# Kernel tuning notes

Measured on AMD Instinct MI355X. Metric: run time of the kernel, lower is better.

Reference implementation:

```python
import jax, jax.numpy as jnp
import numpy as np

D_MODEL = 1024
VOCAB = 32000
NUM_HEADS = 3  # MTP steps
NHEAD = 2      # attention heads per encoder layer
D_FF = 2048    # torch TransformerEncoderLayer default dim_feedforward
EPS_RMS = 1e-8
EPS_LN = 1e-5


def rmsnorm(x):
    rms = jnp.sqrt(jnp.mean(x * x, axis=-1, keepdims=True) + EPS_RMS)
    return x / rms


def layernorm(x, g, b):
    m = jnp.mean(x, axis=-1, keepdims=True)
    v = jnp.mean((x - m) ** 2, axis=-1, keepdims=True)
    return (x - m) / jnp.sqrt(v + EPS_LN) * g + b


def encoder_layer_single_token(x, p):
    # x: (..., d). Self-attention over a length-1 sequence: softmax over one key
    # gives attention weight 1, so attn_out = Wo @ (Wv @ x). Post-norm (torch default).
    v = x @ p['Wv'].T + p['bv']
    attn = v @ p['Wo'].T + p['bo']
    x = layernorm(x + attn, p['ln1_g'], p['ln1_b'])
    ff = jax.nn.relu(x @ p['W1'].T + p['b1']) @ p['W2'].T + p['b2']
    x = layernorm(x + ff, p['ln2_g'], p['ln2_b'])
    return x


def setup_inputs() -> dict:
    key = jax.random.key(0)
    ks = jax.random.split(key, 4)
    token_ids = jax.random.randint(ks[0], (4, 512), 0, VOCAB)
    embed = jax.random.normal(ks[1], (VOCAB, D_MODEL), dtype=jnp.float32) * 0.02
    s = 1.0 / np.sqrt(D_MODEL)
    params = []
    kk = ks[2]
    for k in range(NUM_HEADS):
        kk, *sub = jax.random.split(kk, 10)
        p = {
            'Wmerge': jax.random.normal(sub[0], (D_MODEL, 2 * D_MODEL)) * s,
            'bmerge': jnp.zeros((D_MODEL,)),
            'Wv': jax.random.normal(sub[1], (D_MODEL, D_MODEL)) * s,
            'bv': jnp.zeros((D_MODEL,)),
            'Wo': jax.random.normal(sub[2], (D_MODEL, D_MODEL)) * s,
            'bo': jnp.zeros((D_MODEL,)),
            'W1': jax.random.normal(sub[3], (D_FF, D_MODEL)) * s,
            'b1': jnp.zeros((D_FF,)),
            'W2': jax.random.normal(sub[4], (D_MODEL, D_FF)) * (1.0 / np.sqrt(D_FF)),
            'b2': jnp.zeros((D_MODEL,)),
            'ln1_g': jnp.ones((D_MODEL,)), 'ln1_b': jnp.zeros((D_MODEL,)),
            'ln2_g': jnp.ones((D_MODEL,)), 'ln2_b': jnp.zeros((D_MODEL,)),
        }
        params.append(p)
    # flatten params into dict entries layer{k}_{name}
    out = {'token_ids': token_ids, 'embed': embed}
    for k, p in enumerate(params):
        for name, val in p.items():
            out[f'l{k}_{name}'] = val
    return out


def _forward(token_ids, embed, layers):
    B, T = token_ids.shape
    embeds = embed[token_ids]              # (B, T, d)
    n_pos = T - NUM_HEADS                  # positions i = 0 .. T-NUM_HEADS-1
    # vectorize over i: h_prev starts as h0_seq[:, i, :] for all i at once
    idx = jnp.arange(n_pos)
    h_prev = embeds[:, idx, :]             # (B, P, d)
    logits_list = []
    for k in range(NUM_HEADS):
        p = layers[k]
        tok = embeds[:, idx + (k + 1), :]  # (B, P, d) future token embeds
        merged = jnp.concatenate([rmsnorm(h_prev), rmsnorm(tok)], axis=-1)  # (B,P,2d)
        x = merged @ p['Wmerge'].T + p['bmerge']                            # (B,P,d)
        h_curr = encoder_layer_single_token(x, p)
        logits = h_curr @ embed.T          # tied unembed (B,P,V)
        logits_list.append(logits)
        h_prev = h_curr
    # stack -> (B, P, NUM_HEADS, V) matching torch stack(dim=1) per-position then outer list
    return jnp.stack(logits_list, axis=2)


def reference(token_ids, embed,
              l0_Wmerge, l0_bmerge, l0_Wv, l0_bv, l0_Wo, l0_bo, l0_W1, l0_b1, l0_W2, l0_b2, l0_ln1_g, l0_ln1_b, l0_ln2_g, l0_ln2_b,
              l1_Wmerge, l1_bmerge, l1_Wv, l1_bv, l1_Wo, l1_bo, l1_W1, l1_b1, l1_W2, l1_b2, l1_ln1_g, l1_ln1_b, l1_ln2_g, l1_ln2_b,
              l2_Wmerge, l2_bmerge, l2_Wv, l2_bv, l2_Wo, l2_bo, l2_W1, l2_b1, l2_W2, l2_b2, l2_ln1_g, l2_ln1_b, l2_ln2_g, l2_ln2_b):
    names = ['Wmerge', 'bmerge', 'Wv', 'bv', 'Wo', 'bo', 'W1', 'b1', 'W2', 'b2', 'ln1_g', 'ln1_b', 'ln2_g', 'ln2_b']
    vals = [l0_Wmerge, l0_bmerge, l0_Wv, l0_bv, l0_Wo, l0_bo, l0_W1, l0_b1, l0_W2, l0_b2, l0_ln1_g, l0_ln1_b, l0_ln2_g, l0_ln2_b,
            l1_Wmerge, l1_bmerge, l1_Wv, l1_bv, l1_Wo, l1_bo, l1_W1, l1_b1, l1_W2, l1_b2, l1_ln1_g, l1_ln1_b, l1_ln2_g, l1_ln2_b,
            l2_Wmerge, l2_bmerge, l2_Wv, l2_bv, l2_Wo, l2_bo, l2_W1, l2_b1, l2_W2, l2_b2, l2_ln1_g, l2_ln1_b, l2_ln2_g, l2_ln2_b]
    layers = [dict(zip(names, vals[i * 14:(i + 1) * 14])) for i in range(NUM_HEADS)]
    return _forward(token_ids, embed, layers)
```

## Files before the change

kernel.cpp:

```cpp
#include <hip/hip_runtime.h>


#define NPOS   509
#define MROWS  2036
#define MPAD   2048
#define DMODEL 1024

typedef _Float16 f16;
typedef _Float16 f16x8 __attribute__((ext_vector_type(8)));
typedef _Float16 f16x4 __attribute__((ext_vector_type(4)));
typedef float    f32x4 __attribute__((ext_vector_type(4)));

#define MFMA16(a, b, c) __builtin_amdgcn_mfma_f32_16x16x32_f16(a, b, c, 0, 0, 0)
#define VM0   asm volatile("s_waitcnt vmcnt(0)" ::: "memory")
#define VM2   asm volatile("s_waitcnt vmcnt(2)" ::: "memory")
#define VM4   asm volatile("s_waitcnt vmcnt(4)" ::: "memory")
#define LGKM0 asm volatile("s_waitcnt lgkmcnt(0)" ::: "memory")
#define SCHED0 __builtin_amdgcn_sched_barrier(0)
#define BAR   asm volatile("s_barrier" ::: "memory")

__device__ __forceinline__ void gld_lds16(const void* g, void* l) {
  __builtin_amdgcn_global_load_lds(
      (const __attribute__((address_space(1))) void*)g,
      (__attribute__((address_space(3))) void*)l, 16, 0, 0);
}

__global__ __launch_bounds__(256) void conv_f32_f16(const float* __restrict__ src,
                                                    f16* __restrict__ dst, long n) {
  long i = ((long)blockIdx.x * 256 + threadIdx.x) * 8;
  if (i + 8 <= n) {
    float4 a = *(const float4*)(src + i);
    float4 b = *(const float4*)(src + i + 4);
    f16x8 o = {(f16)a.x, (f16)a.y, (f16)a.z, (f16)a.w,
               (f16)b.x, (f16)b.y, (f16)b.z, (f16)b.w};
    *(f16x8*)(dst + i) = o;
  }
}

struct ConvArgs { const float* s[12]; f16* d[12]; long n[12]; };
__global__ __launch_bounds__(256) void conv_many(ConvArgs a) {
  int t = blockIdx.y;
  long i = ((long)blockIdx.x * 256 + threadIdx.x) * 8;
  if (i + 8 <= a.n[t]) {
    const float* src = a.s[t];
    float4 x = *(const float4*)(src + i);
    float4 y = *(const float4*)(src + i + 4);
    f16x8 o = {(f16)x.x, (f16)x.y, (f16)x.z, (f16)x.w,
               (f16)y.x, (f16)y.y, (f16)y.z, (f16)y.w};
    *(f16x8*)(a.d[t] + i) = o;
  }
}

struct TpArgs { const float* s[3]; f16* d[3]; };
__global__ __launch_bounds__(256) void transpose3(TpArgs a) {
  __shared__ float t[32][33];
  int h = blockIdx.z;
  int bx = blockIdx.x * 32, by = blockIdx.y * 32;
  int tx = threadIdx.x & 31, ty = threadIdx.x >> 5;
  const float* src = a.s[h];
  f16* dst = a.d[h];
  #pragma unroll
  for (int r = 0; r < 32; r += 8)
    t[ty + r][tx] = src[(long)(by + ty + r) * 1024 + bx + tx];
  __syncthreads();
  #pragma unroll
  for (int r = 0; r < 32; r += 8)
    dst[(long)(bx + ty + r) * 1024 + by + tx] = (f16)t[tx][ty + r];
}

struct BvoArgs { const float* Wo[3]; const float* bv[3]; const float* bo[3]; float* out[3]; };
__global__ __launch_bounds__(64) void make_bvo3(BvoArgs a) {
  int h = blockIdx.y, r = blockIdx.x, l = threadIdx.x;
  const float* Wo = a.Wo[h];
  const float* bv = a.bv[h];
  float s = 0.0f;
  for (int k = l; k < 1024; k += 64) s += Wo[(long)r * 1024 + k] * bv[k];
  #pragma unroll
  for (int off = 32; off > 0; off >>= 1) s += __shfl_xor(s, off);
  if (l == 0) a.out[h][r] = s + a.bo[h][r];
}

__device__ __forceinline__ float2 block_reduce2(float a, float b) {
  #pragma unroll
  for (int off = 32; off > 0; off >>= 1) {
    a += __shfl_xor(a, off);
    b += __shfl_xor(b, off);
  }
  __shared__ float2 red[4];
  int wv = threadIdx.x >> 6;
  if ((threadIdx.x & 63) == 0) red[wv] = make_float2(a, b);
  __syncthreads();
  float2 r0 = red[0], r1 = red[1], r2 = red[2], r3 = red[3];
  return make_float2(r0.x + r1.x + r2.x + r3.x, r0.y + r1.y + r2.y + r3.y);
}

__global__ __launch_bounds__(256) void merge_rms(const float* __restrict__ hprev,
                                                 const float* __restrict__ embed,
                                                 const int* __restrict__ tok,
                                                 f16* __restrict__ merged, int koff,
                                                 int hsel) {
  int r = blockIdx.x;
  int b = r / NPOS, t = r - b * NPOS;
  int tid = threadIdx.x;
  const float* hrow = (hsel >= 0)
      ? embed + (long)tok[b * 512 + t + hsel] * DMODEL
      : hprev + (long)r * DMODEL;
  float4 hv = ((const float4*)hrow)[tid];
  float4 tv = ((const float4*)(embed + (long)tok[b * 512 + t + koff] * DMODEL))[tid];
  float sh = hv.x * hv.x + hv.y * hv.y + hv.z * hv.z + hv.w * hv.w;
  float st = tv.x * tv.x + tv.y * tv.y + tv.z * tv.z + tv.w * tv.w;
  float2 tot = block_reduce2(sh, st);
  float ih = 1.0f / sqrtf(tot.x * (1.0f / DMODEL) + 1e-8f);
  float it = 1.0f / sqrtf(tot.y * (1.0f / DMODEL) + 1e-8f);
  f16x4 oh = {(f16)(hv.x * ih), (f16)(hv.y * ih), (f16)(hv.z * ih), (f16)(hv.w * ih)};
  f16x4 ot = {(f16)(tv.x * it), (f16)(tv.y * it), (f16)(tv.z * it), (f16)(tv.w * it)};
  *(f16x4*)(merged + (long)r * 2048 + tid * 4) = oh;
  *(f16x4*)(merged + (long)r * 2048 + 1024 + tid * 4) = ot;
}

__global__ __launch_bounds__(256) void add_ln(const float* __restrict__ x,
                                              const float* __restrict__ res,
                                              const float* __restrict__ g,
                                              const float* __restrict__ bb,
                                              float* __restrict__ yf,
                                              f16* __restrict__ yh) {
  int r = blockIdx.x, tid = threadIdx.x;
  float4 a = ((const float4*)(x + (long)r * DMODEL))[tid];
  float4 c = ((const float4*)(res + (long)r * DMODEL))[tid];
  a.x += c.x; a.y += c.y; a.z += c.z; a.w += c.w;
  float s  = a.x + a.y + a.z + a.w;
  float ss = a.x * a.x + a.y * a.y + a.z * a.z + a.w * a.w;
  float2 tot = block_reduce2(s, ss);
  float mean = tot.x * (1.0f / DMODEL);
  float var  = tot.y * (1.0f / DMODEL) - mean * mean;
  float inv  = 1.0f / sqrtf(var + 1e-5f);
  float4 gv = ((const float4*)g)[tid];
  float4 bv = ((const float4*)bb)[tid];
  float y0 = (a.x - mean) * inv * gv.x + bv.x;
  float y1 = (a.y - mean) * inv * gv.y + bv.y;
  float y2 = (a.z - mean) * inv * gv.z + bv.z;
  float y3 = (a.w - mean) * inv * gv.w + bv.w;
  float4 o = {y0, y1, y2, y3};
  ((float4*)(yf + (long)r * DMODEL))[tid] = o;
  f16x4 oh = {(f16)y0, (f16)y1, (f16)y2, (f16)y3};
  *(f16x4*)(yh + (long)r * DMODEL + tid * 4) = oh;
}

template <int HAS_BIAS, int RELU, int WF32, int WF16, int MASK>
__global__ __launch_bounds__(256) void gemm_sm(const f16* __restrict__ A,
                                               const f16* __restrict__ B,
                                               const float* __restrict__ bias,
                                               float* __restrict__ Cf,
                                               f16* __restrict__ Ch,
                                               int K, int N, long ldc, long coff,
                                               int mval, long zsA, long zsB, long zsC) {
  __shared__ __align__(16) f16 sA[3][2048];
  __shared__ __align__(16) f16 sB[3][2048];
  const int tid  = threadIdx.x;
  const int lane = tid & 63, wv = tid >> 6;
  const int wm = wv >> 1, wn = wv & 1;
  const int bm = blockIdx.y, bn = blockIdx.x;
  const int lr = lane & 15, lk = lane >> 4;

  A += (long)blockIdx.z * zsA;
  B += (long)blockIdx.z * zsB;
  Ch += (long)blockIdx.z * zsC;

  const f16* gA = A + ((long)(bm * 64 + (tid >> 2))) * K + (tid & 3) * 8;
  const f16* gB = B + ((long)(bn * 64 + (tid >> 2))) * K + (tid & 3) * 8;

  const int aoff = (wm * 32 + lr) * 32 + lk * 8;
  const int boff = (wn * 32 + lr) * 32 + lk * 8;

  f32x4 acc[2][2] = {};

#define SSTAGE(buf, kt)                                \
  gld_lds16(gA + (long)(kt) * 32, &sA[buf][tid * 8]);  \
  gld_lds16(gB + (long)(kt) * 32, &sB[buf][tid * 8]);

  const int nk = K >> 5;
  SSTAGE(0, 0);
  SSTAGE(1, 1);

  int cur = 0, stg = 2;
  for (int kt = 0; kt < nk; ++kt) {
    if (kt + 1 < nk) { VM2; } else { VM0; }
    BAR;
    if (kt + 2 < nk) { SSTAGE(stg, kt + 2); }
    f16x8 af0 = *(const f16x8*)&sA[cur][aoff];
    f16x8 af1 = *(const f16x8*)&sA[cur][aoff + 512];
    f16x8 bf0 = *(const f16x8*)&sB[cur][boff];
    f16x8 bf1 = *(const f16x8*)&sB[cur][boff + 512];
    acc[0][0] = MFMA16(af0, bf0, acc[0][0]);
    acc[0][1] = MFMA16(af0, bf1, acc[0][1]);
    acc[1][0] = MFMA16(af1, bf0, acc[1][0]);
    acc[1][1] = MFMA16(af1, bf1, acc[1][1]);
    cur = cur == 2 ? 0 : cur + 1;
    stg = stg == 2 ? 0 : stg + 1;
  }
#undef SSTAGE

  const int row0 = bm * 64 + wm * 32 + lk * 4;
  const int col0 = bn * 64 + wn * 32 + lr;
  #pragma unroll
  for (int mi = 0; mi < 2; ++mi) {
    #pragma unroll
    for (int ni = 0; ni < 2; ++ni) {
      int col = col0 + ni * 16;
      float bs = HAS_BIAS ? bias[col] : 0.0f;
      #pragma unroll
      for (int rg = 0; rg < 4; ++rg) {
        int row = row0 + mi * 16 + rg;
        if (!MASK || row < mval) {
          float v = acc[mi][ni][rg] + bs;
          if (RELU) v = v > 0.0f ? v : 0.0f;
          if (WF32) Cf[(long)row * ldc + coff + col] = v;
          if (WF16) Ch[(long)row * N + col] = (f16)v;
        }
      }
    }
  }
}

__global__ __launch_bounds__(512, 2) void gemm256x(const f16* __restrict__ A,
                                                   const f16* __restrict__ B,
                                                   float* __restrict__ C) {
  __shared__ __align__(16) f16 sA[2][2][8192];
  __shared__ __align__(16) f16 sB[2][2][8192];
  const int K = 1024;
  const int tid = threadIdx.x;
  const int lane = tid & 63;
  const int wv = tid >> 6;
  const int wm = wv >> 2, wn = wv & 3;
  const int lr = lane & 15, lk = lane >> 4;

  const int flat = blockIdx.y * 125 + blockIdx.x;
  const int xcd = flat & 7, i = flat >> 3;
  const int grp = i / 15, w = i % 15;
  const int bm = xcd * 3 + (w % 3);
  const int bn = grp * 5 + (w / 3);

  const int srow = tid >> 2;
  const int schunk = (tid & 3) ^ ((tid >> 3) & 3);
  const f16* gA = A + (long)(bm * 256 + srow) * K + schunk * 8;
  const f16* gB = B + (long)(bn * 256 + srow) * K + schunk * 8;
  const long rstep = 128L * (long)K;

  const int swz = ((lr >> 1) & 3) << 3;
  const int aoff = (((wm * 128 + lr) * 32) + lk * 8) ^ swz;
  const int boff = (((wn * 64  + lr) * 32) + lk * 8) ^ swz;

  f32x4 acc[8][4] = {};

#define STG_A(s, h, ko)                                                  \
  gld_lds16(gA + (ko) + (h) * 32, &sA[s][h][tid * 8]);                   \
  gld_lds16(gA + (ko) + (h) * 32 + rstep, &sA[s][h][tid * 8 + 4096]);
#define STG_B(s, h, ko)                                                  \
  gld_lds16(gB + (ko) + (h) * 32, &sB[s][h][tid * 8]);                   \
  gld_lds16(gB + (ko) + (h) * 32 + rstep, &sB[s][h][tid * 8 + 4096]);

  STG_A(0, 0, 0); STG_B(0, 0, 0); STG_A(0, 1, 0); STG_B(0, 1, 0);
  VM4;
  BAR;

  const int nt = 16;
  for (int t = 0; t < nt; ++t) {
    const int cur = t & 1, nxt = cur ^ 1;
    const long kn = (long)((t + 1 < nt) ? (t + 1) : 0) * 64;
    f16x8 alo[4], ahi[4], bf[4];

    #pragma unroll
    for (int i2 = 0; i2 < 4; ++i2) alo[i2] = *(const f16x8*)&sA[cur][0][aoff + i2 * 512];
    #pragma unroll
    for (int j = 0; j < 4; ++j) bf[j] = *(const f16x8*)&sB[cur][0][boff + j * 512];
    STG_A(nxt, 0, kn);
    BAR; LGKM0; SCHED0;
    __builtin_amdgcn_s_setprio(1);
    #pragma unroll
    for (int i2 = 0; i2 < 4; ++i2)
      #pragma unroll
      for (int j = 0; j < 4; ++j)
        acc[i2][j] = MFMA16(alo[i2], bf[j], acc[i2][j]);
    __builtin_amdgcn_s_setprio(0);
    BAR;

    #pragma unroll
    for (int i2 = 0; i2 < 4; ++i2) ahi[i2] = *(const f16x8*)&sA[cur][0][aoff + (i2 + 4) * 512];
    STG_B(nxt, 0, kn);
    VM4;
    BAR; LGKM0; SCHED0;
    __builtin_amdgcn_s_setprio(1);
    #pragma unroll
    for (int i2 = 0; i2 < 4; ++i2)
      #pragma unroll
      for (int j = 0; j < 4; ++j)
        acc[i2 + 4][j] = MFMA16(ahi[i2], bf[j], acc[i2 + 4][j]);
    __builtin_amdgcn_s_setprio(0);
    BAR;

    #pragma unroll
    for (int i2 = 0; i2 < 4; ++i2) alo[i2] = *(const f16x8*)&sA[cur][1][aoff + i2 * 512];
    #pragma unroll
    for (int j = 0; j < 4; ++j) bf[j] = *(const f16x8*)&sB[cur][1][boff + j * 512];
    STG_A(nxt, 1, kn);
    BAR; LGKM0; SCHED0;
    __builtin_amdgcn_s_setprio(1);
    #pragma unroll
    for (int i2 = 0; i2 < 4; ++i2)
      #pragma unroll
      for (int j = 0; j < 4; ++j)
        acc[i2][j] = MFMA16(alo[i2], bf[j], acc[i2][j]);
    __builtin_amdgcn_s_setprio(0);
    BAR;

    #pragma unroll
    for (int i2 = 0; i2 < 4; ++i2) ahi[i2] = *(const f16x8*)&sA[cur][1][aoff + (i2 + 4) * 512];
    STG_B(nxt, 1, kn);
    VM4;
    BAR; LGKM0; SCHED0;
    __builtin_amdgcn_s_setprio(1);
    #pragma unroll
    for (int i2 = 0; i2 < 4; ++i2)
      #pragma unroll
      for (int j = 0; j < 4; ++j)
        acc[i2 + 4][j] = MFMA16(ahi[i2], bf[j], acc[i2 + 4][j]);
    __builtin_amdgcn_s_setprio(0);
    BAR;
  }
  VM0;

  const int head = bm >> 3;
  const long coff = (long)head * 32000;
  const int row0 = (bm & 7) * 256 + wm * 128 + lk * 4;
  const int col0 = bn * 256 + wn * 64 + lr;
  #pragma unroll
  for (int mi = 0; mi < 8; ++mi) {
    #pragma unroll
    for (int ni = 0; ni < 4; ++ni) {
      int col = col0 + ni * 16;
      #pragma unroll
      for (int rg = 0; rg < 4; ++rg) {
        int row = row0 + mi * 16 + rg;
        if (row < MROWS) C[(long)row * 96000 + coff + col] = acc[mi][ni][rg];
      }
    }
  }
#undef STG_A
#undef STG_B
}

extern "C" void kernel_launch(void* const* d_in, const int* in_sizes, int n_in,
                              void* d_out, int out_size, void* d_ws, size_t ws_size,
                              hipStream_t stream) {
  const int*   tok   = (const int*)d_in[0];
  const float* embed = (const float*)d_in[1];
  auto P = [&](int k, int j) { return (const float*)d_in[2 + k * 14 + j]; };
  float* out = (float*)d_out;

  char* w = (char*)d_ws;
  auto alloc = [&](size_t bytes) { char* p = w; w += bytes; return p; };
  const size_t MM = (size_t)1024 * 1024;

  f16* embed_h = (f16*)alloc((size_t)32000 * 1024 * 2);
  f16* Wo_all  = (f16*)alloc(3 * MM * 2);
  f16* Wvo_all = (f16*)alloc(3 * MM * 2);
  f16 *Wm_h[3], *W1_h[3], *W2_h[3];
  for (int k = 0; k < 3; ++k) {
    Wm_h[k]  = (f16*)alloc((size_t)1024 * 2048 * 2);
    W1_h[k]  = (f16*)alloc((size_t)2048 * 1024 * 2);
    W2_h[k]  = (f16*)alloc((size_t)1024 * 2048 * 2);
  }
  float* hprev  = (float*)alloc((size_t)MPAD * 1024 * 4);
  f16*   h_all  = (f16*)alloc((size_t)3 * MPAD * 1024 * 2);
  f16*   merged = (f16*)alloc((size_t)MPAD * 2048 * 2);
  float* xf     = (float*)alloc((size_t)MPAD * 1024 * 4);
  f16*   xh     = (f16*)alloc((size_t)MPAD * 1024 * 2);
  f16*   ff1    = (f16*)alloc((size_t)MPAD * 2048 * 2);
  float* t1     = (float*)alloc((size_t)MPAD * 1024 * 4);
  float* bvo    = (float*)alloc(3 * 1024 * 4);
  f16* WvT_all = merged;

  conv_f32_f16<<<16000, 256, 0, stream>>>(embed, embed_h, (long)32000 * 1024);

  ConvArgs ca;
  for (int k = 0; k < 3; ++k) {
    ca.s[k*4+0] = P(k, 0); ca.d[k*4+0] = Wm_h[k];        ca.n[k*4+0] = (long)1024 * 2048;
    ca.s[k*4+1] = P(k, 4); ca.d[k*4+1] = Wo_all + k*MM;  ca.n[k*4+1] = (long)1024 * 1024;
    ca.s[k*4+2] = P(k, 6); ca.d[k*4+2] = W1_h[k];        ca.n[k*4+2] = (long)2048 * 1024;
    ca.s[k*4+3] = P(k, 8); ca.d[k*4+3] = W2_h[k];        ca.n[k*4+3] = (long)1024 * 2048;
  }
  conv_many<<<dim3(1024, 12), 256, 0, stream>>>(ca);

  TpArgs ta;
  for (int k = 0; k < 3; ++k) { ta.s[k] = P(k, 2); ta.d[k] = WvT_all + k * MM; }
  transpose3<<<dim3(32, 32, 3), 256, 0, stream>>>(ta);

  gemm_sm<0, 0, 0, 1, 0><<<dim3(16, 16, 3), 256, 0, stream>>>(
      Wo_all, WvT_all, nullptr, nullptr, Wvo_all, 1024, 1024, 1024L, 0L, 1024,
      (long)MM, (long)MM, (long)MM);

  BvoArgs ba;
  for (int k = 0; k < 3; ++k) {
    ba.Wo[k] = P(k, 4); ba.bv[k] = P(k, 3); ba.bo[k] = P(k, 5); ba.out[k] = bvo + k * 1024;
  }
  make_bvo3<<<dim3(1024, 3), 64, 0, stream>>>(ba);

  for (int k = 0; k < 3; ++k) {
    merge_rms<<<MROWS, 256, 0, stream>>>(hprev, embed, tok, merged, k + 1,
                                         k == 0 ? 0 : -1);
    gemm_sm<1, 0, 1, 1, 0><<<dim3(16, 32), 256, 0, stream>>>(
        merged, Wm_h[k], P(k, 1), xf, xh, 2048, 1024, 1024L, 0L, MROWS, 0L, 0L, 0L);
    gemm_sm<1, 0, 1, 0, 0><<<dim3(16, 32), 256, 0, stream>>>(
        xh, Wvo_all + k * MM, bvo + k * 1024, t1, nullptr, 1024, 1024, 1024L, 0L,
        MROWS, 0L, 0L, 0L);
    add_ln<<<MROWS, 256, 0, stream>>>(xf, t1, P(k, 10), P(k, 11), xf, xh);
    gemm_sm<1, 1, 0, 1, 0><<<dim3(32, 32), 256, 0, stream>>>(
        xh, W1_h[k], P(k, 7), nullptr, ff1, 1024, 2048, 2048L, 0L, MROWS, 0L, 0L, 0L);
    gemm_sm<1, 0, 1, 0, 0><<<dim3(16, 32), 256, 0, stream>>>(
        ff1, W2_h[k], P(k, 9), t1, nullptr, 2048, 1024, 1024L, 0L, MROWS, 0L, 0L, 0L);
    add_ln<<<MROWS, 256, 0, stream>>>(xf, t1, P(k, 12), P(k, 13), hprev,
                                      h_all + (size_t)k * MPAD * 1024);
  }

  gemm256x<<<dim3(125, 24), 512, 0, stream>>>(h_all, embed_h, out);
}
```

Measured before the change: 991.6 us.

## Replace 64x64 GEMM with swizzled 128x128-tile kernel using split-phase pipelining

Measured after the change: 1.295 ms. 30.6% more time.

```diff
diff --git a/kernel.cpp b/kernel.cpp
--- a/kernel.cpp
+++ b/kernel.cpp
@@ -13,7 +13,6 @@
 
 #define MFMA16(a, b, c) __builtin_amdgcn_mfma_f32_16x16x32_f16(a, b, c, 0, 0, 0)
 #define VM0   asm volatile("s_waitcnt vmcnt(0)" ::: "memory")
-#define VM2   asm volatile("s_waitcnt vmcnt(2)" ::: "memory")
 #define VM4   asm volatile("s_waitcnt vmcnt(4)" ::: "memory")
 #define LGKM0 asm volatile("s_waitcnt lgkmcnt(0)" ::: "memory")
 #define SCHED0 __builtin_amdgcn_sched_barrier(0)
@@ -146,80 +145,113 @@
   *(f16x4*)(yh + (long)r * DMODEL + tid * 4) = oh;
 }
 
-template <int HAS_BIAS, int RELU, int WF32, int WF16, int MASK>
-__global__ __launch_bounds__(256) void gemm_sm(const f16* __restrict__ A,
-                                               const f16* __restrict__ B,
-                                               const float* __restrict__ bias,
-                                               float* __restrict__ Cf,
-                                               f16* __restrict__ Ch,
-                                               int K, int N, long ldc, long coff,
-                                               int mval, long zsA, long zsB, long zsC) {
-  __shared__ __align__(16) f16 sA[3][2048];
-  __shared__ __align__(16) f16 sB[3][2048];
-  const int tid  = threadIdx.x;
-  const int lane = tid & 63, wv = tid >> 6;
+template <int HAS_BIAS, int RELU, int WF32, int WF16>
+__global__ __launch_bounds__(256, 3) void gemm_md(const f16* __restrict__ A,
+                                                  const f16* __restrict__ B,
+                                                  const float* __restrict__ bias,
+                                                  float* __restrict__ Cf,
+                                                  f16* __restrict__ Ch,
+                                                  int K, int N, long ldc,
+                                                  int mval, long zsA, long zsB, long zsC) {
+  __shared__ __align__(16) f16 sA[3][4096];
+  __shared__ __align__(16) f16 sB[3][4096];
+  const int tid = threadIdx.x;
+  const int lane = tid & 63;
+  const int wv = tid >> 6;
   const int wm = wv >> 1, wn = wv & 1;
+  const int lr = lane & 15, lk = lane >> 4;
   const int bm = blockIdx.y, bn = blockIdx.x;
-  const int lr = lane & 15, lk = lane >> 4;
 
   A += (long)blockIdx.z * zsA;
   B += (long)blockIdx.z * zsB;
   Ch += (long)blockIdx.z * zsC;
 
-  const f16* gA = A + ((long)(bm * 64 + (tid >> 2))) * K + (tid & 3) * 8;
-  const f16* gB = B + ((long)(bn * 64 + (tid >> 2))) * K + (tid & 3) * 8;
-
-  const int aoff = (wm * 32 + lr) * 32 + lk * 8;
-  const int boff = (wn * 32 + lr) * 32 + lk * 8;
-
-  f32x4 acc[2][2] = {};
-
-#define SSTAGE(buf, kt)                                \
-  gld_lds16(gA + (long)(kt) * 32, &sA[buf][tid * 8]);  \
-  gld_lds16(gB + (long)(kt) * 32, &sB[buf][tid * 8]);
-
-  const int nk = K >> 5;
-  SSTAGE(0, 0);
-  SSTAGE(1, 1);
-
-  int cur = 0, stg = 2;
-  for (int kt = 0; kt < nk; ++kt) {
-    if (kt + 1 < nk) { VM2; } else { VM0; }
-    BAR;
-    if (kt + 2 < nk) { SSTAGE(stg, kt + 2); }
-    f16x8 af0 = *(const f16x8*)&sA[cur][aoff];
-    f16x8 af1 = *(const f16x8*)&sA[cur][aoff + 512];
-    f16x8 bf0 = *(const f16x8*)&sB[cur][boff];
-    f16x8 bf1 = *(const f16x8*)&sB[cur][boff + 512];
-    acc[0][0] = MFMA16(af0, bf0, acc[0][0]);
-    acc[0][1] = MFMA16(af0, bf1, acc[0][1]);
-    acc[1][0] = MFMA16(af1, bf0, acc[1][0]);
-    acc[1][1] = MFMA16(af1, bf1, acc[1][1]);
-    cur = cur == 2 ? 0 : cur + 1;
-    stg = stg == 2 ? 0 : stg + 1;
-  }
-#undef SSTAGE
-
-  const int row0 = bm * 64 + wm * 32 + lk * 4;
-  const int col0 = bn * 64 + wn * 32 + lr;
-  #pragma unroll
-  for (int mi = 0; mi < 2; ++mi) {
-    #pragma unroll
-    for (int ni = 0; ni < 2; ++ni) {
+  const int srow = tid >> 2;
+  const int schunk = (tid & 3) ^ ((tid >> 3) & 3);
+  const f16* gA = A + (long)(bm * 128 + srow) * K + schunk * 8;
+  const f16* gB = B + (long)(bn * 128 + srow) * K + schunk * 8;
+
+  const int swz = ((lr >> 1) & 3) << 3;
+  const int aoff = (((wm * 64 + lr) * 32) + lk * 8) ^ swz;
+  const int boff = (((wn * 64 + lr) * 32) + lk * 8) ^ swz;
+
+  f32x4 acc[4][4] = {};
+
+#define STG_A(s, kt, i) gld_lds16(gA + (long)(kt) * 32 + (long)(i) * 64 * K, \
+                                  &sA[s][(i) * 2048 + tid * 8]);
+#define STG_B(s, kt, j) gld_lds16(gB + (long)(kt) * 32 + (long)(j) * 64 * K, \
+                                  &sB[s][(j) * 2048 + tid * 8]);
+#define STAGE_H1(s, kt) STG_A(s, kt, 0) STG_B(s, kt, 0)
+#define STAGE_H2(s, kt) STG_A(s, kt, 1) STG_B(s, kt, 1)
+
+  STAGE_H1(0, 0) STAGE_H2(0, 0)
+  STAGE_H1(1, 1) STAGE_H2(1, 1)
+  VM4; BAR;
+
+  const int nt = K >> 5;
+  int slot = 0;
+  for (int t = 0; t < nt; ++t) {
+    const int s2 = (slot >= 1) ? slot - 1 : slot + 2;
+    const int kt2 = (t + 2 < nt) ? (t + 2) : (t + 2 - nt);
+    f16x8 af[4], bf[4];
+
+    STAGE_H1(s2, kt2)
+    #pragma unroll
+    for (int i = 0; i < 4; ++i) af[i] = *(const f16x8*)&sA[slot][aoff + i * 512];
+    bf[0] = *(const f16x8*)&sB[slot][boff];
+    bf[1] = *(const f16x8*)&sB[slot][boff + 512];
+    LGKM0; SCHED0;
+    __builtin_amdgcn_s_setprio(1);
+    #pragma unroll
+    for (int i = 0; i < 4; ++i) {
+      acc[i][0] = MFMA16(af[i], bf[0], acc[i][0]);
+      acc[i][1] = MFMA16(af[i], bf[1], acc[i][1]);
+    }
+    __builtin_amdgcn_s_setprio(0);
+    BAR;
+
+    STAGE_H2(s2, kt2)
+    bf[2] = *(const f16x8*)&sB[slot][boff + 1024];
+    bf[3] = *(const f16x8*)&sB[slot][boff + 1536];
+    LGKM0; SCHED0;
+    __builtin_amdgcn_s_setprio(1);
+    #pragma unroll
+    for (int i = 0; i < 4; ++i) {
+      acc[i][2] = MFMA16(af[i], bf[2], acc[i][2]);
+      acc[i][3] = MFMA16(af[i], bf[3], acc[i][3]);
+    }
+    __builtin_amdgcn_s_setprio(0);
+    VM4;
+    BAR;
+
+    slot = (slot == 2) ? 0 : slot + 1;
+  }
+  VM0;
+
+  const int row0 = bm * 128 + wm * 64 + lk * 4;
+  const int col0 = bn * 128 + wn * 64 + lr;
+  #pragma unroll
+  for (int mi = 0; mi < 4; ++mi) {
+    #pragma unroll
+    for (int ni = 0; ni < 4; ++ni) {
       int col = col0 + ni * 16;
       float bs = HAS_BIAS ? bias[col] : 0.0f;
       #pragma unroll
       for (int rg = 0; rg < 4; ++rg) {
         int row = row0 + mi * 16 + rg;
-        if (!MASK || row < mval) {
+        if (row < mval) {
           float v = acc[mi][ni][rg] + bs;
           if (RELU) v = v > 0.0f ? v : 0.0f;
-          if (WF32) Cf[(long)row * ldc + coff + col] = v;
+          if (WF32) Cf[(long)row * ldc + col] = v;
           if (WF16) Ch[(long)row * N + col] = (f16)v;
         }
       }
     }
   }
+#undef STG_A
+#undef STG_B
+#undef STAGE_H1
+#undef STAGE_H2
 }
 
 __global__ __launch_bounds__(512, 2) void gemm256x(const f16* __restrict__ A,
@@ -395,8 +427,8 @@
   for (int k = 0; k < 3; ++k) { ta.s[k] = P(k, 2); ta.d[k] = WvT_all + k * MM; }
   transpose3<<<dim3(32, 32, 3), 256, 0, stream>>>(ta);
 
-  gemm_sm<0, 0, 0, 1, 0><<<dim3(16, 16, 3), 256, 0, stream>>>(
-      Wo_all, WvT_all, nullptr, nullptr, Wvo_all, 1024, 1024, 1024L, 0L, 1024,
+  gemm_md<0, 0, 0, 1><<<dim3(8, 8, 3), 256, 0, stream>>>(
+      Wo_all, WvT_all, nullptr, nullptr, Wvo_all, 1024, 1024, 1024L, 1024,
       (long)MM, (long)MM, (long)MM);
 
   BvoArgs ba;
@@ -408,16 +440,16 @@
   for (int k = 0; k < 3; ++k) {
     merge_rms<<<MROWS, 256, 0, stream>>>(hprev, embed, tok, merged, k + 1,
                                          k == 0 ? 0 : -1);
-    gemm_sm<1, 0, 1, 1, 0><<<dim3(16, 32), 256, 0, stream>>>(
-        merged, Wm_h[k], P(k, 1), xf, xh, 2048, 1024, 1024L, 0L, MROWS, 0L, 0L, 0L);
-    gemm_sm<1, 0, 1, 0, 0><<<dim3(16, 32), 256, 0, stream>>>(
-        xh, Wvo_all + k * MM, bvo + k * 1024, t1, nullptr, 1024, 1024, 1024L, 0L,
-        MROWS, 0L, 0L, 0L);
+    gemm_md<1, 0, 1, 1><<<dim3(8, 16), 256, 0, stream>>>(
+        merged, Wm_h[k], P(k, 1), xf, xh, 2048, 1024, 1024L, MPAD, 0L, 0L, 0L);
+    gemm_md<1, 0, 1, 0><<<dim3(8, 16), 256, 0, stream>>>(
+        xh, Wvo_all + k * MM, bvo + k * 1024, t1, nullptr, 1024, 1024, 1024L,
+        MPAD, 0L, 0L, 0L);
     add_ln<<<MROWS, 256, 0, stream>>>(xf, t1, P(k, 10), P(k, 11), xf, xh);
-    gemm_sm<1, 1, 0, 1, 0><<<dim3(32, 32), 256, 0, stream>>>(
-        xh, W1_h[k], P(k, 7), nullptr, ff1, 1024, 2048, 2048L, 0L, MROWS, 0L, 0L, 0L);
-    gemm_sm<1, 0, 1, 0, 0><<<dim3(16, 32), 256, 0, stream>>>(
-        ff1, W2_h[k], P(k, 9), t1, nullptr, 2048, 1024, 1024L, 0L, MROWS, 0L, 0L, 0L);
+    gemm_md<1, 1, 0, 1><<<dim3(16, 16), 256, 0, stream>>>(
+        xh, W1_h[k], P(k, 7), nullptr, ff1, 1024, 2048, 2048L, MPAD, 0L, 0L, 0L);
+    gemm_md<1, 0, 1, 0><<<dim3(8, 16), 256, 0, stream>>>(
+        ff1, W2_h[k], P(k, 9), t1, nullptr, 2048, 1024, 1024L, MPAD, 0L, 0L, 0L);
     add_ln<<<MROWS, 256, 0, stream>>>(xf, t1, P(k, 12), P(k, 13), hprev,
                                       h_all + (size_t)k * MPAD * 1024);
   }
```
